# Kernel optimization log

Hardware: AMD Instinct MI355X
Metric: run time of the kernel (lower is better)

## Reference

```python
import jax, jax.numpy as jnp
import numpy as np

B, S, D = 2, 2048, 1024
H = 16
DH = D // H


def _layernorm(x, g, b, eps=1e-5):
    mu = jnp.mean(x, axis=-1, keepdims=True)
    var = jnp.var(x, axis=-1, keepdims=True)
    return (x - mu) * jax.lax.rsqrt(var + eps) * g + b


def setup_inputs() -> dict:
    key = jax.random.key(0)
    ks = jax.random.split(key, 8)
    s = lambda fan_in: 1.0 / np.sqrt(fan_in)
    return {
        "x": jax.random.normal(ks[0], (B, S, D), dtype=jnp.float32),
        "ln1_g": jnp.ones((D,), jnp.float32),
        "ln1_b": jnp.zeros((D,), jnp.float32),
        "w_qkv": jax.random.uniform(ks[1], (D, 3 * D), jnp.float32, -s(D), s(D)),
        "b_qkv": jnp.zeros((3 * D,), jnp.float32),
        "w_out": jax.random.uniform(ks[2], (D, D), jnp.float32, -s(D), s(D)),
        "b_out": jnp.zeros((D,), jnp.float32),
        "ln2_g": jnp.ones((D,), jnp.float32),
        "ln2_b": jnp.zeros((D,), jnp.float32),
        "w1": jax.random.uniform(ks[3], (D, 4 * D), jnp.float32, -s(D), s(D)),
        "b1": jnp.zeros((4 * D,), jnp.float32),
        "w2": jax.random.uniform(ks[4], (4 * D, D), jnp.float32, -s(4 * D), s(4 * D)),
        "b2": jnp.zeros((D,), jnp.float32),
    }


def reference(x, ln1_g, ln1_b, w_qkv, b_qkv, w_out, b_out,
              ln2_g, ln2_b, w1, b1, w2, b2):
    scale = DH ** -0.5
    residual = x
    h = _layernorm(x, ln1_g, ln1_b)
    qkv = h @ w_qkv + b_qkv                      # [B,S,3D]
    q, k, v = jnp.split(qkv, 3, axis=-1)
    # [B,S,D] -> [B,H,S,DH]
    split_heads = lambda t: t.reshape(B, S, H, DH).transpose(0, 2, 1, 3)
    q, k, v = map(split_heads, (q, k, v))
    scores = jnp.einsum("bhsd,bhtd->bhst", q, k) * scale  # full O(S^2) matrix
    attn = jax.nn.softmax(scores, axis=-1)
    out = jnp.einsum("bhst,bhtd->bhsd", attn, v)
    out = out.transpose(0, 2, 1, 3).reshape(B, S, D)
    out = out @ w_out + b_out                    # dropout is identity at eval
    x = residual + out
    residual = x
    h = _layernorm(x, ln2_g, ln2_b)
    h = jax.nn.gelu(h @ w1 + b1, approximate=False)
    h = h @ w2 + b2
    return residual + h
```

## Files before the change

kernel.cpp:

```cpp
#include <hip/hip_runtime.h>
#include <hip/hip_bf16.h>
#include <math.h>

#define Bc 2
#define Sc 2048
#define Dc 1024
#define Hc 16
#define DHc 64
#define Mc (Bc*Sc)

typedef __attribute__((ext_vector_type(8))) short bf16x8;
typedef __attribute__((ext_vector_type(4))) float f32x4;

#define QSCALE 0.18033688f

__device__ __forceinline__ ushort f2bf(float f){
  union { float f; uint32_t u; } c; c.f = f;
  uint32_t u = c.u;
  return (ushort)((u + 0x7fffu + ((u >> 16) & 1u)) >> 16);
}
__device__ __forceinline__ float fast_exp2(float x){
#if __has_builtin(__builtin_amdgcn_exp2f)
  return __builtin_amdgcn_exp2f(x);
#else
  return exp2f(x);
#endif
}
__device__ __forceinline__ float fast_rcp(float x){
#if __has_builtin(__builtin_amdgcn_rcpf)
  return __builtin_amdgcn_rcpf(x);
#else
  return 1.0f / x;
#endif
}
__device__ __forceinline__ float fast_gelu(float x){
  float x2 = x * x;
  float y  = x * (2.30220826f + 0.10294442f * x2);
  float t  = fast_exp2(fminf(y, 80.f));
  return x * t * fast_rcp(t + 1.0f);
}
__device__ __forceinline__ uint32_t cvt_pk_bf16(float a, float b){
  uint32_t r;
  asm("v_cvt_pk_bf16_f32 %0, %1, %2" : "=v"(r) : "v"(a), "v"(b));
  return r;
}

__device__ __forceinline__ void stage16(const void* g, void* lbase, int lane){
#if __has_builtin(__builtin_amdgcn_global_load_lds)
  __builtin_amdgcn_global_load_lds(
      (const __attribute__((address_space(1))) void*)g,
      (__attribute__((address_space(3))) void*)lbase, 16, 0, 0);
#else
  *(int4*)((char*)lbase + lane*16) = *(const int4*)g;
#endif
}

__global__ __launch_bounds__(256) void tcast(const float* __restrict__ w,
                                             ushort* __restrict__ wt,
                                             int K, int N){
  __shared__ float t[32][33];
  int kb = blockIdx.y * 32, nb = blockIdx.x * 32;
  int tx = threadIdx.x & 31, ty = threadIdx.x >> 5;
  #pragma unroll
  for (int i = 0; i < 4; i++)
    t[ty + 8*i][tx] = w[(size_t)(kb + ty + 8*i) * N + nb + tx];
  __syncthreads();
  #pragma unroll
  for (int i = 0; i < 4; i++)
    wt[(size_t)(nb + ty + 8*i) * K + kb + tx] = f2bf(t[tx][ty + 8*i]);
}

__global__ __launch_bounds__(256) void ln_bf16(const float* __restrict__ x,
                                               const float* __restrict__ g,
                                               const float* __restrict__ b,
                                               ushort* __restrict__ out){
  int row = blockIdx.x;
  const float4 xv = reinterpret_cast<const float4*>(x + (size_t)row * Dc)[threadIdx.x];
  float s  = xv.x + xv.y + xv.z + xv.w;
  float sq = xv.x*xv.x + xv.y*xv.y + xv.z*xv.z + xv.w*xv.w;
  #pragma unroll
  for (int m = 1; m < 64; m <<= 1){ s += __shfl_xor(s, m); sq += __shfl_xor(sq, m); }
  __shared__ float ss[4], ssq[4];
  int wv = threadIdx.x >> 6;
  if ((threadIdx.x & 63) == 0){ ss[wv] = s; ssq[wv] = sq; }
  __syncthreads();
  s  = ss[0] + ss[1] + ss[2] + ss[3];
  sq = ssq[0] + ssq[1] + ssq[2] + ssq[3];
  float mu  = s * (1.0f / Dc);
  float var = sq * (1.0f / Dc) - mu * mu;
  float rstd = rsqrtf(var + 1e-5f);
  float4 gv = reinterpret_cast<const float4*>(g)[threadIdx.x];
  float4 bv = reinterpret_cast<const float4*>(b)[threadIdx.x];
  ushort o[4];
  o[0] = f2bf((xv.x - mu) * rstd * gv.x + bv.x);
  o[1] = f2bf((xv.y - mu) * rstd * gv.y + bv.y);
  o[2] = f2bf((xv.z - mu) * rstd * gv.z + bv.z);
  o[3] = f2bf((xv.w - mu) * rstd * gv.w + bv.w);
  *reinterpret_cast<uint2*>(out + (size_t)row * Dc + threadIdx.x * 4) =
      *reinterpret_cast<uint2*>(o);
}

template<int EPI>
__global__ __launch_bounds__(256) void gemm128(
    const ushort* __restrict__ A, const ushort* __restrict__ BT,
    const float* __restrict__ bias,
    ushort* __restrict__ outb,
    ushort* __restrict__ oq, ushort* __restrict__ ok, ushort* __restrict__ ov,
    int N, int K){
  __shared__ short As[2][128*64];
  __shared__ short Bs[2][128*64];

  const int fid = blockIdx.x;
  const int q8 = gridDim.x >> 3;
  const int id2 = (fid & 7) * q8 + (fid >> 3);
  const int nbx = N / 128;
  const int nb = id2 % nbx, mb = id2 / nbx;

  const int tid = threadIdx.x;
  const int wave = tid >> 6, lane = tid & 63;
  const int wm = wave >> 1, wn = wave & 1;
  const int lr = lane & 15, lg = lane >> 4;

  f32x4 acc[4][4] = {};

  const int srow = wave * 8 + (lane >> 3);
  const int sgc  = ((lane & 7) ^ (lane >> 3)) * 8;
  const ushort* Ag = A  + (size_t)(mb * 128 + srow) * K + sgc;
  const ushort* Bg = BT + (size_t)(nb * 128 + srow) * K + sgc;
  const int nK = K >> 6;

  {
    char* Ab = (char*)&As[0][0] + wave * 1024;
    char* Bb = (char*)&Bs[0][0] + wave * 1024;
    #pragma unroll
    for (int c = 0; c < 4; c++){
      stage16(Ag + (size_t)c * 32 * K, Ab + c * 4096, lane);
      stage16(Bg + (size_t)c * 32 * K, Bb + c * 4096, lane);
    }
  }
  __syncthreads();

  const int swzr = (lr & 7) * 8;

  for (int kt = 0; kt < nK; ++kt){
    const int cur = kt & 1;
    if (kt + 1 < nK){
      const int ko = (kt + 1) * 64;
      char* Ab = (char*)&As[cur ^ 1][0] + wave * 1024;
      char* Bb = (char*)&Bs[cur ^ 1][0] + wave * 1024;
      #pragma unroll
      for (int c = 0; c < 4; c++){
        stage16(Ag + (size_t)c * 32 * K + ko, Ab + c * 4096, lane);
        stage16(Bg + (size_t)c * 32 * K + ko, Bb + c * 4096, lane);
      }
    }
    #pragma unroll
    for (int ks = 0; ks < 2; ks++){
      const int col = (ks * 32 + lg * 8) ^ swzr;
      bf16x8 af[4], bfr[4];
      #pragma unroll
      for (int mt = 0; mt < 4; mt++)
        af[mt] = *reinterpret_cast<const bf16x8*>(&As[cur][(wm*64 + mt*16 + lr)*64 + col]);
      #pragma unroll
      for (int nt = 0; nt < 4; nt++)
        bfr[nt] = *reinterpret_cast<const bf16x8*>(&Bs[cur][(wn*64 + nt*16 + lr)*64 + col]);
      #pragma unroll
      for (int mt = 0; mt < 4; mt++)
        #pragma unroll
        for (int nt = 0; nt < 4; nt++)
          acc[mt][nt] = __builtin_amdgcn_mfma_f32_16x16x32_bf16(af[mt], bfr[nt], acc[mt][nt], 0, 0, 0);
    }
    __syncthreads();
  }

  if (EPI == 0){
    #pragma unroll
    for (int mt = 0; mt < 4; mt++){
      const int gm0 = mb * 128 + wm * 64 + mt * 16 + lg * 4;
      const int bb = gm0 >> 11, s0 = gm0 & 2047;
      #pragma unroll
      for (int nt = 0; nt < 4; nt++){
        const int gn = nb * 128 + wn * 64 + nt * 16 + lr;
        const float bv = bias[gn];
        const int p = gn >> 10, d = gn & 1023;
        const int hh = d >> 6, dh = d & 63;
        const int bh = bb * Hc + hh;
        if (p == 2){
          ushort pk[4];
          #pragma unroll
          for (int r = 0; r < 4; r++) pk[r] = f2bf(acc[mt][nt][r] + bv);
          const int blk = s0 >> 6;
          const int local = s0 & 63;
          const int pos = (local & 32) + ((local & 12) << 1) + ((local & 16) >> 2);
          *reinterpret_cast<uint2*>(ov + ((size_t)bh * DHc + dh) * Sc + blk * 64 + pos) =
              *reinterpret_cast<uint2*>(pk);
        } else if (p == 0){
          #pragma unroll
          for (int r = 0; r < 4; r++)
            oq[((size_t)bh * Sc + s0 + r) * DHc + dh] = f2bf((acc[mt][nt][r] + bv) * QSCALE);
        } else {
          #pragma unroll
          for (int r = 0; r < 4; r++)
            ok[((size_t)bh * Sc + s0 + r) * DHc + dh] = f2bf(acc[mt][nt][r] + bv);
        }
      }
    }
  } else {
    #pragma unroll
    for (int mt = 0; mt < 4; mt++){
      #pragma unroll
      for (int nt = 0; nt < 4; nt++){
        #pragma unroll
        for (int r = 0; r < 4; r++){
          const int gm = mb * 128 + wm * 64 + mt * 16 + lg * 4 + r;
          const int gn = nb * 128 + wn * 64 + nt * 16 + lr;
          outb[(size_t)gm * N + gn] = f2bf(fast_gelu(acc[mt][nt][r] + bias[gn]));
        }
      }
    }
  }
}

__global__ __launch_bounds__(256) void gemm_res64(
    const ushort* __restrict__ A, const ushort* __restrict__ BT,
    const float* __restrict__ bias, const float* __restrict__ res,
    float* __restrict__ outf, int N, int K){
  __shared__ short As[2][128*64];
  __shared__ short Bs[2][64*64];

  const int fid = blockIdx.x;
  const int q8 = gridDim.x >> 3;
  const int id2 = (fid & 7) * q8 + (fid >> 3);
  const int nbx = N / 64;
  const int nb = id2 % nbx, mb = id2 / nbx;

  const int tid = threadIdx.x;
  const int wave = tid >> 6, lane = tid & 63;
  const int wm = wave >> 1, wn = wave & 1;
  const int lr = lane & 15, lg = lane >> 4;

  f32x4 acc[4][2] = {};

  const int srow = wave * 8 + (lane >> 3);
  const int sgc  = ((lane & 7) ^ (lane >> 3)) * 8;
  const ushort* Ag = A  + (size_t)(mb * 128 + srow) * K + sgc;
  const ushort* Bg = BT + (size_t)(nb * 64  + srow) * K + sgc;
  const int nK = K >> 6;

  {
    char* Ab = (char*)&As[0][0] + wave * 1024;
    char* Bb = (char*)&Bs[0][0] + wave * 1024;
    #pragma unroll
    for (int c = 0; c < 4; c++)
      stage16(Ag + (size_t)c * 32 * K, Ab + c * 4096, lane);
    #pragma unroll
    for (int c = 0; c < 2; c++)
      stage16(Bg + (size_t)c * 32 * K, Bb + c * 4096, lane);
  }
  __syncthreads();

  const int swzr = (lr & 7) * 8;

  for (int kt = 0; kt < nK; ++kt){
    const int cur = kt & 1;
    if (kt + 1 < nK){
      const int ko = (kt + 1) * 64;
      char* Ab = (char*)&As[cur ^ 1][0] + wave * 1024;
      char* Bb = (char*)&Bs[cur ^ 1][0] + wave * 1024;
      #pragma unroll
      for (int c = 0; c < 4; c++)
        stage16(Ag + (size_t)c * 32 * K + ko, Ab + c * 4096, lane);
      #pragma unroll
      for (int c = 0; c < 2; c++)
        stage16(Bg + (size_t)c * 32 * K + ko, Bb + c * 4096, lane);
    }
    #pragma unroll
    for (int ks = 0; ks < 2; ks++){
      const int col = (ks * 32 + lg * 8) ^ swzr;
      bf16x8 af[4], bfr[2];
      #pragma unroll
      for (int mt = 0; mt < 4; mt++)
        af[mt] = *reinterpret_cast<const bf16x8*>(&As[cur][(wm*64 + mt*16 + lr)*64 + col]);
      #pragma unroll
      for (int nt = 0; nt < 2; nt++)
        bfr[nt] = *reinterpret_cast<const bf16x8*>(&Bs[cur][(wn*32 + nt*16 + lr)*64 + col]);
      #pragma unroll
      for (int mt = 0; mt < 4; mt++)
        #pragma unroll
        for (int nt = 0; nt < 2; nt++)
          acc[mt][nt] = __builtin_amdgcn_mfma_f32_16x16x32_bf16(af[mt], bfr[nt], acc[mt][nt], 0, 0, 0);
    }
    __syncthreads();
  }

  #pragma unroll
  for (int mt = 0; mt < 4; mt++){
    #pragma unroll
    for (int nt = 0; nt < 2; nt++){
      #pragma unroll
      for (int r = 0; r < 4; r++){
        const int gm = mb * 128 + wm * 64 + mt * 16 + lg * 4 + r;
        const int gn = nb * 64 + wn * 32 + nt * 16 + lr;
        const size_t i = (size_t)gm * N + gn;
        outf[i] = acc[mt][nt][r] + bias[gn] + res[i];
      }
    }
  }
}

__global__ __launch_bounds__(256) void flash_attn(const ushort* __restrict__ q,
                                                  const ushort* __restrict__ k,
                                                  const ushort* __restrict__ vt,
                                                  ushort* __restrict__ ctx){
  const int bh = blockIdx.x;
  const int q0 = blockIdx.y * 64;
  const int b  = bh >> 4, h = bh & 15;
  const int tid = threadIdx.x, wave = tid >> 6, lane = tid & 63;
  const int lr = lane & 15, lg = lane >> 4;

  __shared__ short Kt[2][64*64];
  __shared__ short Vt[2][64*64];

  const int g8  = lane & 7;
  const int kr0 = wave * 8 + (lane >> 3);
  const int kcol = (g8 ^ (kr0 & 7)) * 8;
  const ushort* kg0 = k + (size_t)bh * Sc * DHc + (size_t)kr0 * DHc + kcol;
  const ushort* kg1 = kg0 + 32 * DHc;
  char* Kl = (char*)&Kt[0][0] + wave * 1024;
  const int KBUFB = 64 * 64 * 2;

  const int vrow = tid >> 3, vg8 = tid & 7;
  const int vcol = (vg8 ^ (vrow & 7)) * 8;
  const ushort* vg0 = vt + (size_t)bh * DHc * Sc + (size_t)vrow * Sc + vcol;
  const ushort* vg1 = vg0 + (size_t)32 * Sc;

  bf16x8 qf0, qf1;
  {
    const ushort* qp = q + (size_t)bh * Sc * DHc + (size_t)(q0 + wave * 16 + lr) * DHc + lg * 8;
    qf0 = *reinterpret_cast<const bf16x8*>(qp);
    qf1 = *reinterpret_cast<const bf16x8*>(qp + 32);
  }

  f32x4 o[4] = {};
  float lps = 0.f;
  constexpr int NTILES = Sc / 64;

  stage16(kg0, Kl,        lane);
  stage16(kg1, Kl + 4096, lane);
  {
    int4 w0 = *reinterpret_cast<const int4*>(vg0);
    int4 w1 = *reinterpret_cast<const int4*>(vg1);
    *reinterpret_cast<int4*>((char*)&Vt[0][0] + tid * 16)        = w0;
    *reinterpret_cast<int4*>((char*)&Vt[0][0] + 4096 + tid * 16) = w1;
  }
  __syncthreads();

  const int swz = (lr & 7) * 8;

  for (int kt = 0; kt < NTILES; ++kt){
    const int cur = kt & 1;
    int4 vr0, vr1;
    if (kt + 1 < NTILES){
      const int nx = (cur ^ 1) * KBUFB;
      stage16(kg0 + (size_t)(kt + 1) * 64 * DHc, Kl + nx,        lane);
      stage16(kg1 + (size_t)(kt + 1) * 64 * DHc, Kl + nx + 4096, lane);
      vr0 = *reinterpret_cast<const int4*>(vg0 + (kt + 1) * 64);
      vr1 = *reinterpret_cast<const int4*>(vg1 + (kt + 1) * 64);
    }

    f32x4 sacc[4];
    __builtin_amdgcn_s_setprio(1);
    #pragma unroll
    for (int nt = 0; nt < 4; nt++){
      const int rb = (nt * 16 + lr) * 64;
      bf16x8 b0 = *reinterpret_cast<const bf16x8*>(&Kt[cur][rb + ((lg * 8) ^ swz)]);
      bf16x8 b1 = *reinterpret_cast<const bf16x8*>(&Kt[cur][rb + ((32 + lg * 8) ^ swz)]);
      f32x4 z = {0.f, 0.f, 0.f, 0.f};
      z = __builtin_amdgcn_mfma_f32_16x16x32_bf16(b0, qf0, z, 0, 0, 0);
      z = __builtin_amdgcn_mfma_f32_16x16x32_bf16(b1, qf1, z, 0, 0, 0);
      sacc[nt] = z;
    }
    __builtin_amdgcn_s_setprio(0);

    uint32_t W[4][2];
    #pragma unroll
    for (int nt = 0; nt < 4; nt++){
      float p0 = fast_exp2(sacc[nt][0]);
      float p1 = fast_exp2(sacc[nt][1]);
      float p2 = fast_exp2(sacc[nt][2]);
      float p3 = fast_exp2(sacc[nt][3]);
      lps += (p0 + p1) + (p2 + p3);
      W[nt][0] = cvt_pk_bf16(p0, p1);
      W[nt][1] = cvt_pk_bf16(p2, p3);
    }

    if (kt + 1 < NTILES){
      *reinterpret_cast<int4*>((char*)&Vt[cur ^ 1][0] + tid * 16)        = vr0;
      *reinterpret_cast<int4*>((char*)&Vt[cur ^ 1][0] + 4096 + tid * 16) = vr1;
    }

    union { uint32_t u[4]; bf16x8 v; } c0, c1;
    c0.u[0] = W[0][0]; c0.u[1] = W[0][1]; c0.u[2] = W[1][0]; c0.u[3] = W[1][1];
    c1.u[0] = W[2][0]; c1.u[1] = W[2][1]; c1.u[2] = W[3][0]; c1.u[3] = W[3][1];
    bf16x8 pf0 = c0.v, pf1 = c1.v;

    __builtin_amdgcn_s_setprio(1);
    #pragma unroll
    for (int nt = 0; nt < 4; nt++){
      const int rb = (nt * 16 + lr) * 64;
      bf16x8 v0 = *reinterpret_cast<const bf16x8*>(&Vt[cur][rb + ((lg * 8) ^ swz)]);
      bf16x8 v1 = *reinterpret_cast<const bf16x8*>(&Vt[cur][rb + ((32 + lg * 8) ^ swz)]);
      o[nt] = __builtin_amdgcn_mfma_f32_16x16x32_bf16(pf0, v0, o[nt], 0, 0, 0);
      o[nt] = __builtin_amdgcn_mfma_f32_16x16x32_bf16(pf1, v1, o[nt], 0, 0, 0);
    }
    __builtin_amdgcn_s_setprio(0);

    __syncthreads();
  }

  lps += __shfl_xor(lps, 16);
  lps += __shfl_xor(lps, 32);

  #pragma unroll
  for (int j = 0; j < 4; j++){
    float inv = 1.0f / __shfl(lps, lg * 4 + j);
    int s = q0 + wave * 16 + lg * 4 + j;
    ushort* op = ctx + ((size_t)b * Sc + s) * Dc + h * DHc;
    #pragma unroll
    for (int nt = 0; nt < 4; nt++)
      op[nt * 16 + lr] = f2bf(o[nt][j] * inv);
  }
}

extern "C" void kernel_launch(void* const* d_in, const int* in_sizes, int n_in,
                              void* d_out, int out_size, void* d_ws, size_t ws_size,
                              hipStream_t stream){
  const float* x     = (const float*)d_in[0];
  const float* ln1_g = (const float*)d_in[1];
  const float* ln1_b = (const float*)d_in[2];
  const float* w_qkv = (const float*)d_in[3];
  const float* b_qkv = (const float*)d_in[4];
  const float* w_out = (const float*)d_in[5];
  const float* b_out = (const float*)d_in[6];
  const float* ln2_g = (const float*)d_in[7];
  const float* ln2_b = (const float*)d_in[8];
  const float* w1    = (const float*)d_in[9];
  const float* b1    = (const float*)d_in[10];
  const float* w2    = (const float*)d_in[11];
  const float* b2    = (const float*)d_in[12];
  float* out = (float*)d_out;

  char* ws = (char*)d_ws;
  size_t off = 0;
  ushort* wqkvT = (ushort*)(ws + off); off += (size_t)3072 * 1024 * 2;
  ushort* woutT = (ushort*)(ws + off); off += (size_t)1024 * 1024 * 2;
  ushort* w1T   = (ushort*)(ws + off); off += (size_t)4096 * 1024 * 2;
  ushort* w2T   = (ushort*)(ws + off); off += (size_t)1024 * 4096 * 2;
  ushort* hln   = (ushort*)(ws + off); off += (size_t)Mc * Dc * 2;
  ushort* qbuf  = (ushort*)(ws + off); off += (size_t)32 * Sc * DHc * 2;
  ushort* kbuf  = (ushort*)(ws + off); off += (size_t)32 * Sc * DHc * 2;
  ushort* vtbuf = (ushort*)(ws + off); off += (size_t)32 * Sc * DHc * 2;
  ushort* ctx   = (ushort*)(ws + off); off += (size_t)Mc * Dc * 2;
  float*  x1    = (float*)(ws + off);  off += (size_t)Mc * Dc * 4;
  ushort* act   = qbuf;

  tcast<<<dim3(3072 / 32, 1024 / 32), 256, 0, stream>>>(w_qkv, wqkvT, 1024, 3072);
  tcast<<<dim3(1024 / 32, 1024 / 32), 256, 0, stream>>>(w_out, woutT, 1024, 1024);
  tcast<<<dim3(4096 / 32, 1024 / 32), 256, 0, stream>>>(w1,    w1T,   1024, 4096);
  tcast<<<dim3(1024 / 32, 4096 / 32), 256, 0, stream>>>(w2,    w2T,   4096, 1024);

  ln_bf16<<<Mc, 256, 0, stream>>>(x, ln1_g, ln1_b, hln);

  gemm128<0><<<(3072/128) * (Mc/128), 256, 0, stream>>>(
      hln, wqkvT, b_qkv, nullptr, qbuf, kbuf, vtbuf, 3072, 1024);

  flash_attn<<<dim3(32, Sc / 64), 256, 0, stream>>>(qbuf, kbuf, vtbuf, ctx);

  gemm_res64<<<(1024/64) * (Mc/128), 256, 0, stream>>>(
      ctx, woutT, b_out, x, x1, 1024, 1024);

  ln_bf16<<<Mc, 256, 0, stream>>>(x1, ln2_g, ln2_b, hln);

  gemm128<2><<<(4096/128) * (Mc/128), 256, 0, stream>>>(
      hln, w1T, b1, act, nullptr, nullptr, nullptr, 4096, 1024);

  gemm_res64<<<(1024/64) * (Mc/128), 256, 0, stream>>>(
      act, w2T, b2, x1, out, 1024, 4096);
}
```

Measured before the change: 246.4 us.

## Stage GEMM B tile through registers into a single LDS buffer

The B operand of the 128x128 GEMM no longer uses direct global-to-LDS double buffering. It is loaded into registers during compute and written into a single swizzled LDS buffer after the barrier. This halves LDS use for B, which may allow higher occupancy. The cost is an extra __syncthreads per k-step and more registers, and the B store now sits on the critical path between iterations.

After: 310.5 us. +26.0%, slower.

```diff
diff --git a/kernel.cpp b/kernel.cpp
--- a/kernel.cpp
+++ b/kernel.cpp
@@ -108,7 +108,7 @@
     ushort* __restrict__ oq, ushort* __restrict__ ok, ushort* __restrict__ ov,
     int N, int K){
   __shared__ short As[2][128*64];
-  __shared__ short Bs[2][128*64];
+  __shared__ short Bs[128*64];
 
   const int fid = blockIdx.x;
   const int q8 = gridDim.x >> 3;
@@ -125,18 +125,26 @@
 
   const int srow = wave * 8 + (lane >> 3);
   const int sgc  = ((lane & 7) ^ (lane >> 3)) * 8;
-  const ushort* Ag = A  + (size_t)(mb * 128 + srow) * K + sgc;
-  const ushort* Bg = BT + (size_t)(nb * 128 + srow) * K + sgc;
+  const ushort* Ag = A + (size_t)(mb * 128 + srow) * K + sgc;
+
+  const int brow0 = tid >> 3;
+  const int bgran = tid & 7;
+  const ushort* Bg = BT + (size_t)(nb * 128 + brow0) * K + bgran * 8;
+  const int bws = ((bgran ^ (brow0 & 7)) * 8);
   const int nK = K >> 6;
 
   {
     char* Ab = (char*)&As[0][0] + wave * 1024;
-    char* Bb = (char*)&Bs[0][0] + wave * 1024;
-    #pragma unroll
-    for (int c = 0; c < 4; c++){
+    #pragma unroll
+    for (int c = 0; c < 4; c++)
       stage16(Ag + (size_t)c * 32 * K, Ab + c * 4096, lane);
-      stage16(Bg + (size_t)c * 32 * K, Bb + c * 4096, lane);
-    }
+    int4 br[4];
+    #pragma unroll
+    for (int r = 0; r < 4; r++)
+      br[r] = *reinterpret_cast<const int4*>(Bg + (size_t)r * 32 * K);
+    #pragma unroll
+    for (int r = 0; r < 4; r++)
+      *reinterpret_cast<int4*>(&Bs[(brow0 + r * 32) * 64 + bws]) = br[r];
   }
   __syncthreads();
 
@@ -144,15 +152,16 @@
 
   for (int kt = 0; kt < nK; ++kt){
     const int cur = kt & 1;
+    int4 br[4];
     if (kt + 1 < nK){
       const int ko = (kt + 1) * 64;
       char* Ab = (char*)&As[cur ^ 1][0] + wave * 1024;
-      char* Bb = (char*)&Bs[cur ^ 1][0] + wave * 1024;
-      #pragma unroll
-      for (int c = 0; c < 4; c++){
+      #pragma unroll
+      for (int c = 0; c < 4; c++)
         stage16(Ag + (size_t)c * 32 * K + ko, Ab + c * 4096, lane);
-        stage16(Bg + (size_t)c * 32 * K + ko, Bb + c * 4096, lane);
-      }
+      #pragma unroll
+      for (int r = 0; r < 4; r++)
+        br[r] = *reinterpret_cast<const int4*>(Bg + (size_t)r * 32 * K + ko);
     }
     #pragma unroll
     for (int ks = 0; ks < 2; ks++){
@@ -163,7 +172,7 @@
         af[mt] = *reinterpret_cast<const bf16x8*>(&As[cur][(wm*64 + mt*16 + lr)*64 + col]);
       #pragma unroll
       for (int nt = 0; nt < 4; nt++)
-        bfr[nt] = *reinterpret_cast<const bf16x8*>(&Bs[cur][(wn*64 + nt*16 + lr)*64 + col]);
+        bfr[nt] = *reinterpret_cast<const bf16x8*>(&Bs[(wn*64 + nt*16 + lr)*64 + col]);
       #pragma unroll
       for (int mt = 0; mt < 4; mt++)
         #pragma unroll
@@ -171,6 +180,12 @@
           acc[mt][nt] = __builtin_amdgcn_mfma_f32_16x16x32_bf16(af[mt], bfr[nt], acc[mt][nt], 0, 0, 0);
     }
     __syncthreads();
+    if (kt + 1 < nK){
+      #pragma unroll
+      for (int r = 0; r < 4; r++)
+        *reinterpret_cast<int4*>(&Bs[(brow0 + r * 32) * 64 + bws]) = br[r];
+      __syncthreads();
+    }
   }
 
   if (EPI == 0){
```
